# Kernel tuning notes

Measured on AMD Instinct MI355X. Metric: run time of the kernel, lower is better.

The kernel has to match this reference:

```python
import jax, jax.numpy as jnp
import numpy as np

B, S, D, H = 2, 2048, 2048, 16
HD = D // H  # 128


def _rope(x):
    # x: [b, h, s, d] -- standard half-split rotary embedding, theta=10000
    b, h, s, d = x.shape
    inv_freq = 1.0 / (10000.0 ** (jnp.arange(0, d, 2, dtype=jnp.float32) / d))  # [d/2]
    ang = jnp.arange(s, dtype=jnp.float32)[:, None] * inv_freq[None, :]  # [s, d/2]
    cos = jnp.cos(ang)[None, None].astype(x.dtype)
    sin = jnp.sin(ang)[None, None].astype(x.dtype)
    x1, x2 = x[..., : d // 2], x[..., d // 2 :]
    return jnp.concatenate([x1 * cos - x2 * sin, x2 * cos + x1 * sin], axis=-1)


def setup_inputs() -> dict:
    key = jax.random.key(0)
    ks = jax.random.split(key, 11)
    sc = 0.02
    return {
        "queries": jax.random.normal(ks[0], (B, S, D), jnp.float32),
        "keys": jax.random.normal(ks[1], (B, S, D), jnp.float32),
        "values": jax.random.normal(ks[2], (B, S, D), jnp.float32),
        "Wq": jax.random.normal(ks[3], (D, D), jnp.float32) * sc,
        "bq": jax.random.normal(ks[4], (D,), jnp.float32) * sc,
        "Wk": jax.random.normal(ks[5], (D, D), jnp.float32) * sc,
        "bk": jax.random.normal(ks[6], (D,), jnp.float32) * sc,
        "Wv": jax.random.normal(ks[7], (D, D), jnp.float32) * sc,
        "bv": jax.random.normal(ks[8], (D,), jnp.float32) * sc,
        "Wo": jax.random.normal(ks[9], (D, D), jnp.float32) * sc,
        "bo": jax.random.normal(ks[10], (D,), jnp.float32) * sc,
    }


def reference(queries, keys, values, Wq, bq, Wk, bk, Wv, bv, Wo, bo):
    b, sq, _ = queries.shape
    sk = keys.shape[1]
    # projections, split heads: [b, h, s, hd]
    q = (queries @ Wq + bq).reshape(b, sq, H, HD).transpose(0, 2, 1, 3)
    k = (keys @ Wk + bk).reshape(b, sk, H, HD).transpose(0, 2, 1, 3)
    v = (values @ Wv + bv).reshape(b, sk, H, HD).transpose(0, 2, 1, 3)
    q = _rope(q)
    k = _rope(k)
    scores = jnp.einsum("bhqd,bhkd->bhqk", q, k) / jnp.sqrt(jnp.asarray(HD, q.dtype))
    causal = jnp.triu(jnp.ones((sq, sk), dtype=bool), k=1)
    scores = jnp.where(causal, -jnp.inf, scores)
    attn = jax.nn.softmax(scores, axis=-1)
    out = jnp.einsum("bhqk,bhkd->bhqd", attn, v)
    out = out.transpose(0, 2, 1, 3).reshape(b, sq, H * HD)
    return out @ Wo + bo
```

## Files before the change

kernel.cpp:

```cpp
#include <hip/hip_runtime.h>
#include <hip/hip_bf16.h>
#include <math.h>

#define S_LEN 2048
#define D_DIM 2048
#define NHEAD 16
#define HD_DIM 128
#define NROWS 4096
#define BSD 8388608

typedef __bf16 bf16x8 __attribute__((ext_vector_type(8)));
typedef float f32x4 __attribute__((ext_vector_type(4)));
typedef unsigned short u16;
typedef unsigned int u32;

__device__ __forceinline__ float bf2f(u16 h) {
    union { u32 u; float f; } v; v.u = ((u32)h) << 16; return v.f;
}
__device__ __forceinline__ u16 f2bf(float f) {
    union { float f; u32 u; } v; v.f = f;
    u32 r = v.u + 0x7fffu + ((v.u >> 16) & 1u);
    return (u16)(r >> 16);
}

__device__ __forceinline__ void gld16(const void* g, void* l) {
    __builtin_amdgcn_global_load_lds((const __attribute__((address_space(1))) void*)g,
                                     (__attribute__((address_space(3))) void*)l,
                                     16, 0, 0);
}

__device__ __forceinline__ bool detect_f32(const void* p) {
    const u16* h = (const u16*)p;
    int sane = 0;
    for (int i = 0; i < 128; i++) {
        const u16 v = h[2 * i];
        const int e = (v >> 7) & 0xFF;
        sane += (int)((e >= 96 && e <= 150) || ((v & 0x7FFF) == 0));
    }
    return sane < 64;
}

__device__ __forceinline__ bf16x8 load8(const void* X, size_t eidx, bool f32) {
    if (!f32) return *(const bf16x8*)((const u16*)X + eidx);
    const float* xf = (const float*)X + eidx;
    const f32x4 a = *(const f32x4*)xf;
    const f32x4 b = *(const f32x4*)(xf + 4);
    bf16x8 r;
    u16* rp = (u16*)&r;
    rp[0] = f2bf(a[0]); rp[1] = f2bf(a[1]); rp[2] = f2bf(a[2]); rp[3] = f2bf(a[3]);
    rp[4] = f2bf(b[0]); rp[5] = f2bf(b[1]); rp[6] = f2bf(b[2]); rp[7] = f2bf(b[3]);
    return r;
}

__device__ __forceinline__ float bload(const void* b, int i, bool f32) {
    return f32 ? ((const float*)b)[i] : bf2f(((const u16*)b)[i]);
}

__global__ __launch_bounds__(256) void fill_k(float* __restrict__ out, float v, int n) {
    const int i = blockIdx.x * 256 + threadIdx.x;
    if (i < n) out[i] = v;
}

__device__ __forceinline__ void conv_body(const void* __restrict__ in,
                                          u16* __restrict__ out, bool f32) {
    const size_t i = ((size_t)blockIdx.x * 256 + threadIdx.x) << 3;
    if (f32) {
        const f32x4 a = *(const f32x4*)((const float*)in + i);
        const f32x4 b = *(const f32x4*)((const float*)in + i + 4);
        uint4 w;
        w.x = (u32)f2bf(a[0]) | ((u32)f2bf(a[1]) << 16);
        w.y = (u32)f2bf(a[2]) | ((u32)f2bf(a[3]) << 16);
        w.z = (u32)f2bf(b[0]) | ((u32)f2bf(b[1]) << 16);
        w.w = (u32)f2bf(b[2]) | ((u32)f2bf(b[3]) << 16);
        *(uint4*)&out[i] = w;
    } else {
        *(uint4*)&out[i] = *(const uint4*)&((const u16*)in)[i];
    }
}

__global__ __launch_bounds__(256) void conv_bf16(const void* __restrict__ in,
                                                 u16* __restrict__ out) {
    conv_body(in, out, detect_f32(in));
}

__global__ __launch_bounds__(256) void conv3(const void* __restrict__ q,
                                             const void* __restrict__ k,
                                             const void* __restrict__ v,
                                             u16* __restrict__ oq,
                                             u16* __restrict__ ok,
                                             u16* __restrict__ ov) {
    const int z = blockIdx.y;
    const void* in = (z == 0) ? q : (z == 1) ? k : v;
    u16* out = (z == 0) ? oq : (z == 1) ? ok : ov;
    conv_body(in, out, detect_f32(in));
}

__device__ __forceinline__ void transpose_body(const void* __restrict__ W,
                                               u16* __restrict__ out) {
    __shared__ float tile[64][68];
    const bool f32w = detect_f32(W);
    const int t = threadIdx.x;
    const int r = t >> 4, c4 = (t & 15) << 2;
    const int kb = blockIdx.y << 6, nb = blockIdx.x << 6;
    if (f32w) {
        #pragma unroll
        for (int i = 0; i < 4; i++) {
            const f32x4 v = *(const f32x4*)((const float*)W +
                (size_t)(kb + r + 16 * i) * D_DIM + nb + c4);
            tile[r + 16 * i][c4 + 0] = v[0];
            tile[r + 16 * i][c4 + 1] = v[1];
            tile[r + 16 * i][c4 + 2] = v[2];
            tile[r + 16 * i][c4 + 3] = v[3];
        }
    } else {
        #pragma unroll
        for (int i = 0; i < 4; i++)
            #pragma unroll
            for (int j = 0; j < 4; j++)
                tile[r + 16 * i][c4 + j] =
                    bf2f(((const u16*)W)[(size_t)(kb + r + 16 * i) * D_DIM + nb + c4 + j]);
    }
    __syncthreads();
    #pragma unroll
    for (int i = 0; i < 4; i++) {
        const int n = nb + r + 16 * i;
        u16 pk[4];
        #pragma unroll
        for (int j = 0; j < 4; j++) pk[j] = f2bf(tile[c4 + j][r + 16 * i]);
        *(uint2*)&out[(size_t)n * D_DIM + kb + c4] = *(uint2*)pk;
    }
}

__global__ __launch_bounds__(256) void transpose_w(const void* __restrict__ W,
                                                   u16* __restrict__ out) {
    transpose_body(W, out);
}

__global__ __launch_bounds__(256) void transpose_all(const void* __restrict__ W0,
                                                     const void* __restrict__ W1,
                                                     const void* __restrict__ W2,
                                                     u16* __restrict__ out) {
    const int z = blockIdx.z;
    const void* W = (z == 0) ? W0 : (z == 1) ? W1 : W2;
    transpose_body(W, out + (size_t)z * D_DIM * D_DIM);
}

__global__ __launch_bounds__(256) void qkv_gemm_bf(const u16* __restrict__ Xq,
                                                   const u16* __restrict__ Xk,
                                                   const u16* __restrict__ Xv,
                                                   const u16* __restrict__ WTbase,
                                                   const void* __restrict__ bqp,
                                                   const void* __restrict__ bkp,
                                                   const void* __restrict__ bvp,
                                                   u16* __restrict__ Oq,
                                                   u16* __restrict__ Ok,
                                                   u16* __restrict__ Ov) {
    __shared__ __align__(16) u16 a_s[128 * 32];
    __shared__ __align__(16) u16 b_s[128 * 32];
    const int z = blockIdx.z;
    const u16* X    = (z == 0) ? Xq  : (z == 1) ? Xk  : Xv;
    const void* bias= (z == 0) ? bqp : (z == 1) ? bkp : bvp;
    u16* out        = (z == 0) ? Oq  : (z == 1) ? Ok  : Ov;
    const u16* WT   = WTbase + (size_t)z * D_DIM * D_DIM;
    const bool f32b = detect_f32(bias);
    const int t = threadIdx.x;
    const int wave = t >> 6, lane = t & 63;
    const int quad = lane >> 4, m16 = lane & 15;
    const int wm = (wave >> 1) << 6, wn = (wave & 1) << 6;
    const int rowBase = blockIdx.y << 7, colBase = blockIdx.x << 7;
    const int arow = t >> 2, aoff = (t & 3) << 3;

    f32x4 acc[4][4];
    #pragma unroll
    for (int i = 0; i < 4; i++)
        #pragma unroll
        for (int j = 0; j < 4; j++) acc[i][j] = (f32x4){0.f, 0.f, 0.f, 0.f};

    for (int k0 = 0; k0 < D_DIM; k0 += 32) {
        __syncthreads();
        gld16(&X[(size_t)(rowBase + arow) * D_DIM + k0 + aoff],       &a_s[t * 8]);
        gld16(&X[(size_t)(rowBase + arow + 64) * D_DIM + k0 + aoff],  &a_s[(t + 256) * 8]);
        gld16(&WT[(size_t)(colBase + arow) * D_DIM + k0 + aoff],      &b_s[t * 8]);
        gld16(&WT[(size_t)(colBase + arow + 64) * D_DIM + k0 + aoff], &b_s[(t + 256) * 8]);
        __syncthreads();

        bf16x8 af[4], bfr[4];
        #pragma unroll
        for (int mi = 0; mi < 4; mi++)
            af[mi] = *(bf16x8*)&a_s[(wm + mi * 16 + m16) * 32 + quad * 8];
        #pragma unroll
        for (int ni = 0; ni < 4; ni++)
            bfr[ni] = *(bf16x8*)&b_s[(wn + ni * 16 + m16) * 32 + quad * 8];
        #pragma unroll
        for (int mi = 0; mi < 4; mi++)
            #pragma unroll
            for (int ni = 0; ni < 4; ni++)
                acc[mi][ni] = __builtin_amdgcn_mfma_f32_16x16x32_bf16(
                    af[mi], bfr[ni], acc[mi][ni], 0, 0, 0);
    }

    #pragma unroll
    for (int ni = 0; ni < 4; ni++) {
        const int col = colBase + wn + ni * 16 + m16;
        const float bv = bload(bias, col, f32b);
        const int h = col >> 7, hd = col & (HD_DIM - 1);
        #pragma unroll
        for (int mi = 0; mi < 4; mi++) {
            #pragma unroll
            for (int r = 0; r < 4; r++) {
                const int row = rowBase + wm + mi * 16 + quad * 4 + r;
                const int b = row >> 11, s = row & (S_LEN - 1);
                out[(((size_t)(b * NHEAD + h)) * S_LEN + s) * HD_DIM + hd] =
                    f2bf(acc[mi][ni][r] + bv);
            }
        }
    }
}

__global__ __launch_bounds__(256) void qkv_gemm(const void* __restrict__ Xq,
                                                const void* __restrict__ Xk,
                                                const void* __restrict__ Xv,
                                                const u16* __restrict__ WTbase,
                                                const void* __restrict__ bqp,
                                                const void* __restrict__ bkp,
                                                const void* __restrict__ bvp,
                                                u16* __restrict__ Oq,
                                                u16* __restrict__ Ok,
                                                u16* __restrict__ Ov) {
    __shared__ __align__(16) u16 a_s[128 * 32];
    __shared__ __align__(16) u16 b_s[128 * 32];
    const int z = blockIdx.z;
    const void* X   = (z == 0) ? Xq  : (z == 1) ? Xk  : Xv;
    const void* bias= (z == 0) ? bqp : (z == 1) ? bkp : bvp;
    u16* out        = (z == 0) ? Oq  : (z == 1) ? Ok  : Ov;
    const u16* WT   = WTbase + (size_t)z * D_DIM * D_DIM;
    const bool f32x = detect_f32(X);
    const bool f32b = detect_f32(bias);
    const int t = threadIdx.x;
    const int wave = t >> 6, lane = t & 63;
    const int quad = lane >> 4, m16 = lane & 15;
    const int wm = (wave >> 1) << 6, wn = (wave & 1) << 6;
    const int rowBase = blockIdx.y << 7, colBase = blockIdx.x << 7;
    const int arow = t >> 2, aoff = (t & 3) << 3;

    f32x4 acc[4][4];
    #pragma unroll
    for (int i = 0; i < 4; i++)
        #pragma unroll
        for (int j = 0; j < 4; j++) acc[i][j] = (f32x4){0.f, 0.f, 0.f, 0.f};

    for (int k0 = 0; k0 < D_DIM; k0 += 32) {
        const bf16x8 av0 = load8(X, (size_t)(rowBase + arow) * D_DIM + k0 + aoff, f32x);
        const bf16x8 av1 = load8(X, (size_t)(rowBase + arow + 64) * D_DIM + k0 + aoff, f32x);
        __syncthreads();
        *(bf16x8*)&a_s[arow * 32 + aoff]        = av0;
        *(bf16x8*)&a_s[(arow + 64) * 32 + aoff] = av1;
        gld16(&WT[(size_t)(colBase + arow) * D_DIM + k0 + aoff],      &b_s[t * 8]);
        gld16(&WT[(size_t)(colBase + arow + 64) * D_DIM + k0 + aoff], &b_s[(t + 256) * 8]);
        __syncthreads();

        bf16x8 af[4], bfr[4];
        #pragma unroll
        for (int mi = 0; mi < 4; mi++)
            af[mi] = *(bf16x8*)&a_s[(wm + mi * 16 + m16) * 32 + quad * 8];
        #pragma unroll
        for (int ni = 0; ni < 4; ni++)
            bfr[ni] = *(bf16x8*)&b_s[(wn + ni * 16 + m16) * 32 + quad * 8];
        #pragma unroll
        for (int mi = 0; mi < 4; mi++)
            #pragma unroll
            for (int ni = 0; ni < 4; ni++)
                acc[mi][ni] = __builtin_amdgcn_mfma_f32_16x16x32_bf16(
                    af[mi], bfr[ni], acc[mi][ni], 0, 0, 0);
    }

    #pragma unroll
    for (int ni = 0; ni < 4; ni++) {
        const int col = colBase + wn + ni * 16 + m16;
        const float bv = bload(bias, col, f32b);
        const int h = col >> 7, hd = col & (HD_DIM - 1);
        #pragma unroll
        for (int mi = 0; mi < 4; mi++) {
            #pragma unroll
            for (int r = 0; r < 4; r++) {
                const int row = rowBase + wm + mi * 16 + quad * 4 + r;
                const int b = row >> 11, s = row & (S_LEN - 1);
                out[(((size_t)(b * NHEAD + h)) * S_LEN + s) * HD_DIM + hd] =
                    f2bf(acc[mi][ni][r] + bv);
            }
        }
    }
}

template<int MODE>
__global__ __launch_bounds__(256) void bt_gemm(const void* __restrict__ X,
                                               const u16* __restrict__ WT,
                                               const void* __restrict__ bias,
                                               void* __restrict__ out) {
    __shared__ __align__(16) u16 a_s[128 * 32];
    __shared__ __align__(16) u16 b_s[128 * 32];
    const bool f32x = (MODE == 0) ? detect_f32(X) : false;
    const bool f32b = detect_f32(bias);
    const int t = threadIdx.x;
    const int wave = t >> 6, lane = t & 63;
    const int quad = lane >> 4, m16 = lane & 15;
    const int wm = (wave >> 1) << 6, wn = (wave & 1) << 6;
    const int rowBase = blockIdx.y << 7, colBase = blockIdx.x << 7;
    const int arow = t >> 2, aoff = (t & 3) << 3;

    f32x4 acc[4][4];
    #pragma unroll
    for (int i = 0; i < 4; i++)
        #pragma unroll
        for (int j = 0; j < 4; j++) acc[i][j] = (f32x4){0.f, 0.f, 0.f, 0.f};

    for (int k0 = 0; k0 < D_DIM; k0 += 32) {
        if (MODE == 0) {
            const bf16x8 av0 = load8(X, (size_t)(rowBase + arow) * D_DIM + k0 + aoff, f32x);
            const bf16x8 av1 = load8(X, (size_t)(rowBase + arow + 64) * D_DIM + k0 + aoff, f32x);
            __syncthreads();
            *(bf16x8*)&a_s[arow * 32 + aoff]        = av0;
            *(bf16x8*)&a_s[(arow + 64) * 32 + aoff] = av1;
            gld16(&WT[(size_t)(colBase + arow) * D_DIM + k0 + aoff],      &b_s[t * 8]);
            gld16(&WT[(size_t)(colBase + arow + 64) * D_DIM + k0 + aoff], &b_s[(t + 256) * 8]);
            __syncthreads();
        } else {
            __syncthreads();
            if (MODE == 2) {
                gld16(&((const u16*)X)[(size_t)(rowBase + arow) * D_DIM + k0 + aoff],
                      &a_s[t * 8]);
                gld16(&((const u16*)X)[(size_t)(rowBase + arow + 64) * D_DIM + k0 + aoff],
                      &a_s[(t + 256) * 8]);
            } else {
                const int kg = k0 + aoff, h = kg >> 7, hd = kg & (HD_DIM - 1);
                const int r0 = rowBase + arow, r1 = r0 + 64;
                gld16(&((const u16*)X)[
                    (((size_t)((r0 >> 11) * NHEAD + h)) * S_LEN + (r0 & (S_LEN - 1))) * HD_DIM + hd],
                    &a_s[t * 8]);
                gld16(&((const u16*)X)[
                    (((size_t)((r1 >> 11) * NHEAD + h)) * S_LEN + (r1 & (S_LEN - 1))) * HD_DIM + hd],
                    &a_s[(t + 256) * 8]);
            }
            gld16(&WT[(size_t)(colBase + arow) * D_DIM + k0 + aoff],      &b_s[t * 8]);
            gld16(&WT[(size_t)(colBase + arow + 64) * D_DIM + k0 + aoff], &b_s[(t + 256) * 8]);
            __syncthreads();
        }

        bf16x8 af[4], bfr[4];
        #pragma unroll
        for (int mi = 0; mi < 4; mi++)
            af[mi] = *(bf16x8*)&a_s[(wm + mi * 16 + m16) * 32 + quad * 8];
        #pragma unroll
        for (int ni = 0; ni < 4; ni++)
            bfr[ni] = *(bf16x8*)&b_s[(wn + ni * 16 + m16) * 32 + quad * 8];
        #pragma unroll
        for (int mi = 0; mi < 4; mi++)
            #pragma unroll
            for (int ni = 0; ni < 4; ni++)
                acc[mi][ni] = __builtin_amdgcn_mfma_f32_16x16x32_bf16(
                    af[mi], bfr[ni], acc[mi][ni], 0, 0, 0);
    }

    #pragma unroll
    for (int ni = 0; ni < 4; ni++) {
        const int col = colBase + wn + ni * 16 + m16;
        const float bv = bload(bias, col, f32b);
        const int h = col >> 7, hd = col & (HD_DIM - 1);
        #pragma unroll
        for (int mi = 0; mi < 4; mi++) {
            #pragma unroll
            for (int r = 0; r < 4; r++) {
                const int row = rowBase + wm + mi * 16 + quad * 4 + r;
                const float v = acc[mi][ni][r] + bv;
                if (MODE == 1) {
                    ((float*)out)[(size_t)row * D_DIM + col] = v;
                } else {
                    const int b = row >> 11, s = row & (S_LEN - 1);
                    ((u16*)out)[(((size_t)(b * NHEAD + h)) * S_LEN + s) * HD_DIM + hd] = f2bf(v);
                }
            }
        }
    }
}

__global__ __launch_bounds__(256) void gemm_qkv(const void* __restrict__ X,
                                                const void* __restrict__ W,
                                                const void* __restrict__ bias,
                                                u16* __restrict__ out) {
    __shared__ __align__(16) u16 a_s[64 * 32];
    __shared__ __align__(16) u16 b_s[64 * 40];
    const bool f32x = detect_f32(X);
    const bool f32w = detect_f32(W);
    const bool f32b = detect_f32(bias);
    const int t = threadIdx.x;
    const int wave = t >> 6, lane = t & 63;
    const int quad = lane >> 4, mrow = lane & 15;
    const int rowBase = blockIdx.y * 64;
    const int colBase = blockIdx.x * 64;
    const int srow = t >> 2, soff = (t & 3) << 3;
    const int krow = t >> 3, ncol0 = (t & 7) << 3;

    f32x4 acc0 = {0.f, 0.f, 0.f, 0.f};
    f32x4 acc1 = acc0, acc2 = acc0, acc3 = acc0;

    for (int k0 = 0; k0 < D_DIM; k0 += 32) {
        const bf16x8 av = load8(X, (size_t)(rowBase + srow) * D_DIM + k0 + soff, f32x);
        const bf16x8 wv = load8(W, (size_t)(k0 + krow) * D_DIM + colBase + ncol0, f32w);
        __syncthreads();
        *(bf16x8*)&a_s[srow * 32 + soff] = av;
        const u16* wp = (const u16*)&wv;
        #pragma unroll
        for (int j = 0; j < 8; j++) b_s[(ncol0 + j) * 40 + krow] = wp[j];
        __syncthreads();
        const bf16x8 af  = *(bf16x8*)&a_s[(wave * 16 + mrow) * 32 + (quad << 3)];
        const bf16x8 bf0 = *(bf16x8*)&b_s[(     mrow) * 40 + (quad << 3)];
        const bf16x8 bf1 = *(bf16x8*)&b_s[(16 + mrow) * 40 + (quad << 3)];
        const bf16x8 bf2 = *(bf16x8*)&b_s[(32 + mrow) * 40 + (quad << 3)];
        const bf16x8 bf3 = *(bf16x8*)&b_s[(48 + mrow) * 40 + (quad << 3)];
        acc0 = __builtin_amdgcn_mfma_f32_16x16x32_bf16(af, bf0, acc0, 0, 0, 0);
        acc1 = __builtin_amdgcn_mfma_f32_16x16x32_bf16(af, bf1, acc1, 0, 0, 0);
        acc2 = __builtin_amdgcn_mfma_f32_16x16x32_bf16(af, bf2, acc2, 0, 0, 0);
        acc3 = __builtin_amdgcn_mfma_f32_16x16x32_bf16(af, bf3, acc3, 0, 0, 0);
    }

    const f32x4 accs[4] = {acc0, acc1, acc2, acc3};
    #pragma unroll
    for (int cb = 0; cb < 4; cb++) {
        const int col = colBase + cb * 16 + mrow;
        const float bv = bload(bias, col, f32b);
        const int h = col >> 7, hd = col & (HD_DIM - 1);
        #pragma unroll
        for (int r = 0; r < 4; r++) {
            const int row = rowBase + wave * 16 + quad * 4 + r;
            const int b = row >> 11, s = row & (S_LEN - 1);
            out[(((size_t)(b * NHEAD + h)) * S_LEN + s) * HD_DIM + hd] =
                f2bf(accs[cb][r] + bv);
        }
    }
}

__global__ __launch_bounds__(256) void gemm_o(const u16* __restrict__ A,
                                              const void* __restrict__ W,
                                              const void* __restrict__ bias,
                                              float* __restrict__ out) {
    __shared__ __align__(16) u16 a_s[64 * 32];
    __shared__ __align__(16) u16 b_s[64 * 40];
    const bool f32w = detect_f32(W);
    const bool f32b = detect_f32(bias);
    const int t = threadIdx.x;
    const int wave = t >> 6, lane = t & 63;
    const int quad = lane >> 4, mrow = lane & 15;
    const int rowBase = blockIdx.y * 64;
    const int colBase = blockIdx.x * 64;
    const int srow = t >> 2, soff = (t & 3) << 3;
    const int krow = t >> 3, ncol0 = (t & 7) << 3;

    f32x4 acc0 = {0.f, 0.f, 0.f, 0.f};
    f32x4 acc1 = acc0, acc2 = acc0, acc3 = acc0;

    const int row = rowBase + srow;
    const int rb = row >> 11, rs = row & (S_LEN - 1);

    for (int k0 = 0; k0 < D_DIM; k0 += 32) {
        const int kg = k0 + soff;
        const int h = kg >> 7, hd = kg & (HD_DIM - 1);
        const bf16x8 av = *(const bf16x8*)&A[
            (((size_t)(rb * NHEAD + h)) * S_LEN + rs) * HD_DIM + hd];
        const bf16x8 wv = load8(W, (size_t)(k0 + krow) * D_DIM + colBase + ncol0, f32w);
        __syncthreads();
        *(bf16x8*)&a_s[srow * 32 + soff] = av;
        const u16* wp = (const u16*)&wv;
        #pragma unroll
        for (int j = 0; j < 8; j++) b_s[(ncol0 + j) * 40 + krow] = wp[j];
        __syncthreads();
        const bf16x8 af  = *(bf16x8*)&a_s[(wave * 16 + mrow) * 32 + (quad << 3)];
        const bf16x8 bf0 = *(bf16x8*)&b_s[(     mrow) * 40 + (quad << 3)];
        const bf16x8 bf1 = *(bf16x8*)&b_s[(16 + mrow) * 40 + (quad << 3)];
        const bf16x8 bf2 = *(bf16x8*)&b_s[(32 + mrow) * 40 + (quad << 3)];
        const bf16x8 bf3 = *(bf16x8*)&b_s[(48 + mrow) * 40 + (quad << 3)];
        acc0 = __builtin_amdgcn_mfma_f32_16x16x32_bf16(af, bf0, acc0, 0, 0, 0);
        acc1 = __builtin_amdgcn_mfma_f32_16x16x32_bf16(af, bf1, acc1, 0, 0, 0);
        acc2 = __builtin_amdgcn_mfma_f32_16x16x32_bf16(af, bf2, acc2, 0, 0, 0);
        acc3 = __builtin_amdgcn_mfma_f32_16x16x32_bf16(af, bf3, acc3, 0, 0, 0);
    }

    const f32x4 accs[4] = {acc0, acc1, acc2, acc3};
    #pragma unroll
    for (int cb = 0; cb < 4; cb++) {
        const int col = colBase + cb * 16 + mrow;
        const float bv = bload(bias, col, f32b);
        #pragma unroll
        for (int r = 0; r < 4; r++) {
            const int orow = rowBase + wave * 16 + quad * 4 + r;
            out[(size_t)orow * D_DIM + col] = accs[cb][r] + bv;
        }
    }
}

__global__ __launch_bounds__(256) void rope_k(u16* __restrict__ q, u16* __restrict__ k) {
    const int idx = blockIdx.x * 256 + threadIdx.x;
    u16* p = blockIdx.y ? k : q;
    const int i  = idx & 63;
    const int s  = (idx >> 6) & (S_LEN - 1);
    const int bh = idx >> 17;
    const size_t base = ((size_t)bh * S_LEN + s) * HD_DIM;
    const float inv = __expf((float)i * -0.14391157f);
    const float ang = (float)s * inv;
    const float c = cosf(ang), sn = sinf(ang);
    const float x1 = bf2f(p[base + i]);
    const float x2 = bf2f(p[base + 64 + i]);
    p[base + i]      = f2bf(x1 * c - x2 * sn);
    p[base + 64 + i] = f2bf(x2 * c + x1 * sn);
}

__device__ __forceinline__ int vswz(int d, int blk8) {
    return d * 72 + (((blk8) ^ ((d ^ (d >> 3)) & 7)) << 3);
}

__global__ __launch_bounds__(256, 3) void flash_mfma(const u16* Q,
                                                     const u16* __restrict__ K,
                                                     const u16* __restrict__ V,
                                                     u16* Out) {
    __shared__ __align__(16) u16 k_s[64 * 136];
    __shared__ __align__(16) u16 v_s[128 * 72];
    __shared__ __align__(16) u16 p_s[64 * 72];
    const int t = threadIdx.x;
    const int wave = t >> 6, lane = t & 63;
    const int quad = lane >> 4, m16 = lane & 15;
    const int h = blockIdx.y, b = blockIdx.z;
    const int q0 = (int)(gridDim.x - 1 - blockIdx.x) << 6;
    const size_t bhoff = ((size_t)(b * NHEAD + h)) * S_LEN * HD_DIM;

    #pragma unroll
    for (int i = 0; i < 4; i++) {
        const int chunk = t + 256 * i;
        const int row = chunk >> 4, d0 = (chunk & 15) << 3;
        *(uint4*)&k_s[row * 136 + d0] =
            *(const uint4*)&Q[bhoff + (size_t)(q0 + row) * HD_DIM + d0];
    }
    __syncthreads();
    bf16x8 qf[4];
    #pragma unroll
    for (int kc = 0; kc < 4; kc++)
        qf[kc] = *(bf16x8*)&k_s[(wave * 16 + m16) * 136 + kc * 32 + quad * 8];

    f32x4 o[8];
    #pragma unroll
    for (int i = 0; i < 8; i++) o[i] = (f32x4){0.f, 0.f, 0.f, 0.f};
    f32x4 m_i = {-1e30f, -1e30f, -1e30f, -1e30f};
    f32x4 l_i = {0.f, 0.f, 0.f, 0.f};

    const int row_g0 = q0 + wave * 16 + quad * 4;
    const float scale = 0.08838834764831843f;
    const int nt = (q0 >> 6) + 1;

    const int krow = t >> 4, kd0 = (t & 15) << 3;
    const int dg = t & 15, kvg = t >> 4;
    const int vsub = (kvg & 1) << 2;

    uint4 kreg[4], vreg[4];
    #pragma unroll
    for (int i = 0; i < 4; i++) {
        kreg[i] = *(const uint4*)&K[bhoff + (size_t)(krow + 16 * i) * HD_DIM + kd0];
        vreg[i] = *(const uint4*)&V[bhoff + (size_t)(kvg * 4 + i) * HD_DIM + dg * 8];
    }

    for (int it = 0; it < nt; ++it) {
        const int kb = it << 6;
        __syncthreads();
        #pragma unroll
        for (int i = 0; i < 4; i++)
            *(uint4*)&k_s[(krow + 16 * i) * 136 + kd0] = kreg[i];
        {
            const u16* v0 = (const u16*)&vreg[0];
            const u16* v1 = (const u16*)&vreg[1];
            const u16* v2 = (const u16*)&vreg[2];
            const u16* v3 = (const u16*)&vreg[3];
            #pragma unroll
            for (int j = 0; j < 8; j++) {
                const int d = dg * 8 + j;
                uint2 w;
                w.x = (u32)v0[j] | ((u32)v1[j] << 16);
                w.y = (u32)v2[j] | ((u32)v3[j] << 16);
                *(uint2*)&v_s[vswz(d, kvg >> 1) + vsub] = w;
            }
        }
        __syncthreads();
        if (it + 1 < nt) {
            const int kb2 = kb + 64;
            #pragma unroll
            for (int i = 0; i < 4; i++) {
                kreg[i] = *(const uint4*)&K[bhoff + (size_t)(kb2 + krow + 16 * i) * HD_DIM + kd0];
                vreg[i] = *(const uint4*)&V[bhoff + (size_t)(kb2 + kvg * 4 + i) * HD_DIM + dg * 8];
            }
        }

        f32x4 s[4];
        #pragma unroll
        for (int f = 0; f < 4; f++) s[f] = (f32x4){0.f, 0.f, 0.f, 0.f};
        __builtin_amdgcn_s_setprio(1);
        #pragma unroll
        for (int kc = 0; kc < 4; kc++) {
            #pragma unroll
            for (int f = 0; f < 4; f++) {
                const bf16x8 kf = *(bf16x8*)&k_s[(f * 16 + m16) * 136 + kc * 32 + quad * 8];
                s[f] = __builtin_amdgcn_mfma_f32_16x16x32_bf16(qf[kc], kf, s[f], 0, 0, 0);
            }
        }
        __builtin_amdgcn_s_setprio(0);

        f32x4 mx;
        #pragma unroll
        for (int r = 0; r < 4; r++) {
            float m0 = -1e30f;
            #pragma unroll
            for (int f = 0; f < 4; f++) {
                float a = s[f][r] * scale;
                if (kb + f * 16 + m16 > row_g0 + r) a = -1e30f;
                s[f][r] = a;
                m0 = fmaxf(m0, a);
            }
            mx[r] = m0;
        }
        #pragma unroll
        for (int d = 1; d <= 8; d <<= 1)
            #pragma unroll
            for (int r = 0; r < 4; r++) mx[r] = fmaxf(mx[r], __shfl_xor(mx[r], d));

        f32x4 alpha, rs;
        #pragma unroll
        for (int r = 0; r < 4; r++) {
            const float mn = fmaxf(m_i[r], mx[r]);
            alpha[r] = __expf(m_i[r] - mn);
            m_i[r] = mn;
            float acc = 0.f;
            #pragma unroll
            for (int f = 0; f < 4; f++) {
                s[f][r] = __expf(s[f][r] - mn);
                acc += s[f][r];
            }
            rs[r] = acc;
        }
        #pragma unroll
        for (int d = 1; d <= 8; d <<= 1)
            #pragma unroll
            for (int r = 0; r < 4; r++) rs[r] += __shfl_xor(rs[r], d);
        #pragma unroll
        for (int r = 0; r < 4; r++) l_i[r] = l_i[r] * alpha[r] + rs[r];

        #pragma unroll
        for (int f = 0; f < 4; f++)
            #pragma unroll
            for (int r = 0; r < 4; r++)
                p_s[(wave * 16 + quad * 4 + r) * 72 + f * 16 + m16] = f2bf(s[f][r]);

        #pragma unroll
        for (int n = 0; n < 8; n++) o[n] *= alpha;

        __builtin_amdgcn_s_setprio(1);
        #pragma unroll
        for (int kc = 0; kc < 2; kc++) {
            const bf16x8 pa = *(bf16x8*)&p_s[(wave * 16 + m16) * 72 + kc * 32 + quad * 8];
            #pragma unroll
            for (int n = 0; n < 8; n++) {
                const int d = n * 16 + m16;
                const bf16x8 vb = *(bf16x8*)&v_s[vswz(d, kc * 4 + quad)];
                o[n] = __builtin_amdgcn_mfma_f32_16x16x32_bf16(pa, vb, o[n], 0, 0, 0);
            }
        }
        __builtin_amdgcn_s_setprio(0);
    }

    f32x4 inv;
    #pragma unroll
    for (int r = 0; r < 4; r++) inv[r] = 1.f / l_i[r];
    #pragma unroll
    for (int n = 0; n < 8; n++)
        #pragma unroll
        for (int r = 0; r < 4; r++)
            Out[bhoff + (size_t)(row_g0 + r) * HD_DIM + n * 16 + m16] =
                f2bf(o[n][r] * inv[r]);
}

extern "C" void kernel_launch(void* const* d_in, const int* in_sizes, int n_in,
                              void* d_out, int out_size, void* d_ws, size_t ws_size,
                              hipStream_t stream) {
    float* outf = (float*)d_out;

    bool order_ok = (n_in == 11);
    if (order_ok) {
        const int expect[11] = {8388608, 8388608, 8388608, 4194304, 2048,
                                4194304, 2048, 4194304, 2048, 4194304, 2048};
        for (int i = 0; i < 11; i++) order_ok = order_ok && (in_sizes[i] == expect[i]);
    }
    if (!order_ok) {
        fill_k<<<dim3((out_size + 255) / 256), dim3(256), 0, stream>>>(outf, 50.f, out_size);
        return;
    }
    if (ws_size < (size_t)BSD * sizeof(u16)) {
        fill_k<<<dim3((out_size + 255) / 256), dim3(256), 0, stream>>>(outf, 25.f, out_size);
        return;
    }

    const void* queries = d_in[0];
    const void* keys    = d_in[1];
    const void* values  = d_in[2];
    const void* Wq = d_in[3]; const void* bq = d_in[4];
    const void* Wk = d_in[5]; const void* bk = d_in[6];
    const void* Wv = d_in[7]; const void* bv = d_in[8];
    const void* Wo = d_in[9]; const void* bo = d_in[10];

    const dim3 tb(256);
    const dim3 gr(16384, 2);
    const dim3 gf(S_LEN / 64, NHEAD, 2);

    const size_t wslot = (size_t)D_DIM * D_DIM * 2;
    const size_t need_full  = (size_t)BSD * 8 + 3 * wslot;
    const size_t need_fused = (size_t)BSD * 4 + 3 * wslot;
    const size_t need_fast  = (size_t)BSD * 4 + wslot;

    if (ws_size >= need_full) {
        u16* Qb = (u16*)d_ws;
        u16* Kb = Qb + BSD;
        u16* Vb = Kb + BSD;
        u16* WT = Vb + BSD;
        u16* XV = WT + 3 * (size_t)D_DIM * D_DIM;
        u16* XQ = (u16*)d_out;
        u16* XK = XQ + BSD;

        const dim3 gc3(4096, 3);
        const dim3 gt3(32, 32, 3);
        const dim3 gt(32, 32);
        const dim3 gq(16, 32, 3);
        const dim3 gb(16, 32);

        conv3<<<gc3, tb, 0, stream>>>(queries, keys, values, XQ, XK, XV);
        transpose_all<<<gt3, tb, 0, stream>>>(Wq, Wk, Wv, WT);
        qkv_gemm_bf<<<gq, tb, 0, stream>>>(XQ, XK, XV, WT, bq, bk, bv, Qb, Kb, Vb);
        transpose_w<<<gt, tb, 0, stream>>>(Wo, WT);
        rope_k<<<gr, tb, 0, stream>>>(Qb, Kb);
        flash_mfma<<<gf, tb, 0, stream>>>(Qb, Kb, Vb, Qb);
        bt_gemm<1><<<gb, tb, 0, stream>>>(Qb, WT, bo, outf);
        return;
    }

    u16* Qb = (u16*)d_ws;
    u16* Kb = (u16*)d_out;
    u16* Vb = Kb + BSD;

    const size_t need_r3 = (size_t)BSD * 2 + 3 * wslot;
    const size_t need_r2 = (size_t)BSD * 2 + wslot;

    if (ws_size >= need_r3) {
        u16* WT = Qb + BSD;
        const dim3 gt3(32, 32, 3);
        const dim3 gt(32, 32);
        const dim3 gq(16, 32, 3);
        const dim3 gb(16, 32);

        transpose_all<<<gt3, tb, 0, stream>>>(Wq, Wk, Wv, WT);
        qkv_gemm<<<gq, tb, 0, stream>>>(queries, keys, values, WT,
                                        bq, bk, bv, Qb, Kb, Vb);
        transpose_w<<<gt, tb, 0, stream>>>(Wo, WT);
        rope_k<<<gr, tb, 0, stream>>>(Qb, Kb);
        flash_mfma<<<gf, tb, 0, stream>>>(Qb, Kb, Vb, Qb);
        bt_gemm<1><<<gb, tb, 0, stream>>>(Qb, WT, bo, outf);
    } else if (ws_size >= need_r2) {
        u16* WT = Qb + BSD;
        u16* XQ = Kb;
        u16* XK = Vb;
        const dim3 gt(32, 32);
        const dim3 gb(16, 32);
        const dim3 gc(4096);

        conv_bf16<<<gc, tb, 0, stream>>>(queries, XQ);
        conv_bf16<<<gc, tb, 0, stream>>>(keys, XK);

        transpose_w<<<gt, tb, 0, stream>>>(Wq, WT);
        bt_gemm<2><<<gb, tb, 0, stream>>>(XQ, WT, bq, Qb);
        transpose_w<<<gt, tb, 0, stream>>>(Wk, WT);
        bt_gemm<2><<<gb, tb, 0, stream>>>(XK, WT, bk, Kb);
        transpose_w<<<gt, tb, 0, stream>>>(Wv, WT);
        bt_gemm<0><<<gb, tb, 0, stream>>>(values, WT, bv, Vb);

        rope_k<<<gr, tb, 0, stream>>>(Qb, Kb);
        flash_mfma<<<gf, tb, 0, stream>>>(Qb, Kb, Vb, Qb);

        transpose_w<<<gt, tb, 0, stream>>>(Wo, WT);
        bt_gemm<1><<<gb, tb, 0, stream>>>(Qb, WT, bo, outf);
    } else {
        const dim3 gg(32, 64);
        gemm_qkv<<<gg, tb, 0, stream>>>(queries, Wq, bq, Qb);
        gemm_qkv<<<gg, tb, 0, stream>>>(keys,    Wk, bk, Kb);
        gemm_qkv<<<gg, tb, 0, stream>>>(values,  Wv, bv, Vb);
        rope_k<<<gr, tb, 0, stream>>>(Qb, Kb);
        flash_mfma<<<gf, tb, 0, stream>>>(Qb, Kb, Vb, Qb);
        gemm_o<<<gg, tb, 0, stream>>>(Qb, Wo, bo, outf);
    }
}
```

Baseline: 829.1 us.

## Double-buffer GEMM LDS tiles and add 8-wave 128-row flash attention kernel

The QKV and output-projection GEMMs now use two LDS buffers, so the async global-to-LDS loads for the next K slice are issued before the MFMA work on the current slice, with one barrier per iteration instead of two. A new flash attention kernel uses 512 threads covering 128 query rows per block, sharing each staged K/V tile across twice as many rows. It also prefetches the next K/V tile into registers and uses reversed block order to schedule the longer causal rows first. The costs are doubled LDS use in the GEMMs and higher register and LDS pressure in the attention kernel, which may lower occupancy. In the attention kernel, the Q/K/V buffer is also overwritten with the output in place.

```diff
diff --git a/kernel.cpp b/kernel.cpp
--- a/kernel.cpp
+++ b/kernel.cpp
@@ -155,8 +155,8 @@
                                                    u16* __restrict__ Oq,
                                                    u16* __restrict__ Ok,
                                                    u16* __restrict__ Ov) {
-    __shared__ __align__(16) u16 a_s[128 * 32];
-    __shared__ __align__(16) u16 b_s[128 * 32];
+    __shared__ __align__(16) u16 a_s[2][128 * 32];
+    __shared__ __align__(16) u16 b_s[2][128 * 32];
     const int z = blockIdx.z;
     const u16* X    = (z == 0) ? Xq  : (z == 1) ? Xk  : Xv;
     const void* bias= (z == 0) ? bqp : (z == 1) ? bkp : bvp;
@@ -176,27 +176,35 @@
         #pragma unroll
         for (int j = 0; j < 4; j++) acc[i][j] = (f32x4){0.f, 0.f, 0.f, 0.f};
 
-    for (int k0 = 0; k0 < D_DIM; k0 += 32) {
-        __syncthreads();
-        gld16(&X[(size_t)(rowBase + arow) * D_DIM + k0 + aoff],       &a_s[t * 8]);
-        gld16(&X[(size_t)(rowBase + arow + 64) * D_DIM + k0 + aoff],  &a_s[(t + 256) * 8]);
-        gld16(&WT[(size_t)(colBase + arow) * D_DIM + k0 + aoff],      &b_s[t * 8]);
-        gld16(&WT[(size_t)(colBase + arow + 64) * D_DIM + k0 + aoff], &b_s[(t + 256) * 8]);
-        __syncthreads();
-
+    gld16(&X[(size_t)(rowBase + arow) * D_DIM + aoff],        &a_s[0][t * 8]);
+    gld16(&X[(size_t)(rowBase + arow + 64) * D_DIM + aoff],   &a_s[0][(t + 256) * 8]);
+    gld16(&WT[(size_t)(colBase + arow) * D_DIM + aoff],       &b_s[0][t * 8]);
+    gld16(&WT[(size_t)(colBase + arow + 64) * D_DIM + aoff],  &b_s[0][(t + 256) * 8]);
+    __syncthreads();
+
+    int cur = 0;
+    for (int k0 = 0; k0 < D_DIM; k0 += 32, cur ^= 1) {
+        if (k0 + 32 < D_DIM) {
+            const int kn = k0 + 32;
+            gld16(&X[(size_t)(rowBase + arow) * D_DIM + kn + aoff],       &a_s[cur ^ 1][t * 8]);
+            gld16(&X[(size_t)(rowBase + arow + 64) * D_DIM + kn + aoff],  &a_s[cur ^ 1][(t + 256) * 8]);
+            gld16(&WT[(size_t)(colBase + arow) * D_DIM + kn + aoff],      &b_s[cur ^ 1][t * 8]);
+            gld16(&WT[(size_t)(colBase + arow + 64) * D_DIM + kn + aoff], &b_s[cur ^ 1][(t + 256) * 8]);
+        }
         bf16x8 af[4], bfr[4];
         #pragma unroll
         for (int mi = 0; mi < 4; mi++)
-            af[mi] = *(bf16x8*)&a_s[(wm + mi * 16 + m16) * 32 + quad * 8];
+            af[mi] = *(bf16x8*)&a_s[cur][(wm + mi * 16 + m16) * 32 + quad * 8];
         #pragma unroll
         for (int ni = 0; ni < 4; ni++)
-            bfr[ni] = *(bf16x8*)&b_s[(wn + ni * 16 + m16) * 32 + quad * 8];
+            bfr[ni] = *(bf16x8*)&b_s[cur][(wn + ni * 16 + m16) * 32 + quad * 8];
         #pragma unroll
         for (int mi = 0; mi < 4; mi++)
             #pragma unroll
             for (int ni = 0; ni < 4; ni++)
                 acc[mi][ni] = __builtin_amdgcn_mfma_f32_16x16x32_bf16(
                     af[mi], bfr[ni], acc[mi][ni], 0, 0, 0);
+        __syncthreads();
     }
 
     #pragma unroll
@@ -297,9 +305,6 @@
                                                const u16* __restrict__ WT,
                                                const void* __restrict__ bias,
                                                void* __restrict__ out) {
-    __shared__ __align__(16) u16 a_s[128 * 32];
-    __shared__ __align__(16) u16 b_s[128 * 32];
-    const bool f32x = (MODE == 0) ? detect_f32(X) : false;
     const bool f32b = detect_f32(bias);
     const int t = threadIdx.x;
     const int wave = t >> 6, lane = t & 63;
@@ -314,8 +319,11 @@
         #pragma unroll
         for (int j = 0; j < 4; j++) acc[i][j] = (f32x4){0.f, 0.f, 0.f, 0.f};
 
-    for (int k0 = 0; k0 < D_DIM; k0 += 32) {
-        if (MODE == 0) {
+    if constexpr (MODE == 0) {
+        __shared__ __align__(16) u16 a_s[128 * 32];
+        __shared__ __align__(16) u16 b_s[128 * 32];
+        const bool f32x = detect_f32(X);
+        for (int k0 = 0; k0 < D_DIM; k0 += 32) {
             const bf16x8 av0 = load8(X, (size_t)(rowBase + arow) * D_DIM + k0 + aoff, f32x);
             const bf16x8 av1 = load8(X, (size_t)(rowBase + arow + 64) * D_DIM + k0 + aoff, f32x);
             __syncthreads();
@@ -324,41 +332,66 @@
             gld16(&WT[(size_t)(colBase + arow) * D_DIM + k0 + aoff],      &b_s[t * 8]);
             gld16(&WT[(size_t)(colBase + arow + 64) * D_DIM + k0 + aoff], &b_s[(t + 256) * 8]);
             __syncthreads();
-        } else {
+
+            bf16x8 af[4], bfr[4];
+            #pragma unroll
+            for (int mi = 0; mi < 4; mi++)
+                af[mi] = *(bf16x8*)&a_s[(wm + mi * 16 + m16) * 32 + quad * 8];
+            #pragma unroll
+            for (int ni = 0; ni < 4; ni++)
+                bfr[ni] = *(bf16x8*)&b_s[(wn + ni * 16 + m16) * 32 + quad * 8];
+            #pragma unroll
+            for (int mi = 0; mi < 4; mi++)
+                #pragma unroll
+                for (int ni = 0; ni < 4; ni++)
+                    acc[mi][ni] = __builtin_amdgcn_mfma_f32_16x16x32_bf16(
+                        af[mi], bfr[ni], acc[mi][ni], 0, 0, 0);
+        }
+    } else {
+        __shared__ __align__(16) u16 a_s[2][128 * 32];
+        __shared__ __align__(16) u16 b_s[2][128 * 32];
+        #define STAGE_T(buf, kk)                                                          \
+            do {                                                                          \
+                if (MODE == 2) {                                                          \
+                    gld16(&((const u16*)X)[(size_t)(rowBase + arow) * D_DIM + (kk) + aoff],      \
+                          &a_s[buf][t * 8]);                                              \
+                    gld16(&((const u16*)X)[(size_t)(rowBase + arow + 64) * D_DIM + (kk) + aoff], \
+                          &a_s[buf][(t + 256) * 8]);                                      \
+                } else {                                                                  \
+                    const int kg = (kk) + aoff, hh = kg >> 7, hd2 = kg & (HD_DIM - 1);    \
+                    const int r0 = rowBase + arow, r1 = r0 + 64;                          \
+                    gld16(&((const u16*)X)[                                               \
+                        (((size_t)((r0 >> 11) * NHEAD + hh)) * S_LEN + (r0 & (S_LEN - 1))) * HD_DIM + hd2], \
+                        &a_s[buf][t * 8]);                                                \
+                    gld16(&((const u16*)X)[                                               \
+                        (((size_t)((r1 >> 11) * NHEAD + hh)) * S_LEN + (r1 & (S_LEN - 1))) * HD_DIM + hd2], \
+                        &a_s[buf][(t + 256) * 8]);                                        \
+                }                                                                         \
+                gld16(&WT[(size_t)(colBase + arow) * D_DIM + (kk) + aoff],      &b_s[buf][t * 8]);        \
+                gld16(&WT[(size_t)(colBase + arow + 64) * D_DIM + (kk) + aoff], &b_s[buf][(t + 256) * 8]);\
+            } while (0)
+
+        STAGE_T(0, 0);
+        __syncthreads();
+        int cur = 0;
+        for (int k0 = 0; k0 < D_DIM; k0 += 32, cur ^= 1) {
+            if (k0 + 32 < D_DIM) STAGE_T(cur ^ 1, k0 + 32);
+            bf16x8 af[4], bfr[4];
+            #pragma unroll
+            for (int mi = 0; mi < 4; mi++)
+                af[mi] = *(bf16x8*)&a_s[cur][(wm + mi * 16 + m16) * 32 + quad * 8];
+            #pragma unroll
+            for (int ni = 0; ni < 4; ni++)
+                bfr[ni] = *(bf16x8*)&b_s[cur][(wn + ni * 16 + m16) * 32 + quad * 8];
+            #pragma unroll
+            for (int mi = 0; mi < 4; mi++)
+                #pragma unroll
+                for (int ni = 0; ni < 4; ni++)
+                    acc[mi][ni] = __builtin_amdgcn_mfma_f32_16x16x32_bf16(
+                        af[mi], bfr[ni], acc[mi][ni], 0, 0, 0);
             __syncthreads();
-            if (MODE == 2) {
-                gld16(&((const u16*)X)[(size_t)(rowBase + arow) * D_DIM + k0 + aoff],
-                      &a_s[t * 8]);
-                gld16(&((const u16*)X)[(size_t)(rowBase + arow + 64) * D_DIM + k0 + aoff],
-                      &a_s[(t + 256) * 8]);
-            } else {
-                const int kg = k0 + aoff, h = kg >> 7, hd = kg & (HD_DIM - 1);
-                const int r0 = rowBase + arow, r1 = r0 + 64;
-                gld16(&((const u16*)X)[
-                    (((size_t)((r0 >> 11) * NHEAD + h)) * S_LEN + (r0 & (S_LEN - 1))) * HD_DIM + hd],
-                    &a_s[t * 8]);
-                gld16(&((const u16*)X)[
-                    (((size_t)((r1 >> 11) * NHEAD + h)) * S_LEN + (r1 & (S_LEN - 1))) * HD_DIM + hd],
-                    &a_s[(t + 256) * 8]);
-            }
-            gld16(&WT[(size_t)(colBase + arow) * D_DIM + k0 + aoff],      &b_s[t * 8]);
-            gld16(&WT[(size_t)(colBase + arow + 64) * D_DIM + k0 + aoff], &b_s[(t + 256) * 8]);
-            __syncthreads();
-        }
-
-        bf16x8 af[4], bfr[4];
-        #pragma unroll
-        for (int mi = 0; mi < 4; mi++)
-            af[mi] = *(bf16x8*)&a_s[(wm + mi * 16 + m16) * 32 + quad * 8];
-        #pragma unroll
-        for (int ni = 0; ni < 4; ni++)
-            bfr[ni] = *(bf16x8*)&b_s[(wn + ni * 16 + m16) * 32 + quad * 8];
-        #pragma unroll
-        for (int mi = 0; mi < 4; mi++)
-            #pragma unroll
-            for (int ni = 0; ni < 4; ni++)
-                acc[mi][ni] = __builtin_amdgcn_mfma_f32_16x16x32_bf16(
-                    af[mi], bfr[ni], acc[mi][ni], 0, 0, 0);
+        }
+        #undef STAGE_T
     }
 
     #pragma unroll
@@ -682,6 +715,173 @@
                 f2bf(o[n][r] * inv[r]);
 }
 
+__global__ __launch_bounds__(512, 4) void flash_mfma8(const u16* __restrict__ Q,
+                                                      const u16* __restrict__ K,
+                                                      const u16* __restrict__ V,
+                                                      u16* __restrict__ Out) {
+    __shared__ __align__(16) u16 k_s[64 * 136];
+    __shared__ __align__(16) u16 v_s[128 * 72];
+    __shared__ __align__(16) u16 p_s[128 * 72];
+    const int t = threadIdx.x;
+    const int wave = t >> 6, lane = t & 63;
+    const int quad = lane >> 4, m16 = lane & 15;
+    const int h = blockIdx.y, b = blockIdx.z;
+    const int q0 = (int)(gridDim.x - 1 - blockIdx.x) << 7;
+    const size_t bhoff = ((size_t)(b * NHEAD + h)) * S_LEN * HD_DIM;
+
+    bf16x8 qf[4];
+    {
+        const size_t qrow = bhoff + (size_t)(q0 + wave * 16 + m16) * HD_DIM;
+        #pragma unroll
+        for (int kc = 0; kc < 4; kc++)
+            qf[kc] = *(const bf16x8*)&Q[qrow + kc * 32 + quad * 8];
+    }
+
+    f32x4 o[8];
+    #pragma unroll
+    for (int i = 0; i < 8; i++) o[i] = (f32x4){0.f, 0.f, 0.f, 0.f};
+    f32x4 m_i = {-1e30f, -1e30f, -1e30f, -1e30f};
+    f32x4 l_i = {0.f, 0.f, 0.f, 0.f};
+
+    const int row_g0 = q0 + wave * 16 + quad * 4;
+    const float scale = 0.08838834764831843f;
+    const int nt = (q0 >> 6) + 2;
+
+    const int krow = t >> 4, kd0 = (t & 15) << 3;
+    const int dg = t & 15, kvp = t >> 4;
+    const int vbase = (kvp & 3) << 1;
+
+    uint4 kreg[2], vreg[2];
+    kreg[0] = *(const uint4*)&K[bhoff + (size_t)(krow) * HD_DIM + kd0];
+    kreg[1] = *(const uint4*)&K[bhoff + (size_t)(krow + 32) * HD_DIM + kd0];
+    vreg[0] = *(const uint4*)&V[bhoff + (size_t)(kvp * 2) * HD_DIM + dg * 8];
+    vreg[1] = *(const uint4*)&V[bhoff + (size_t)(kvp * 2 + 1) * HD_DIM + dg * 8];
+
+    for (int it = 0; it < nt; ++it) {
+        const int kb = it << 6;
+        __syncthreads();
+        *(uint4*)&k_s[(krow) * 136 + kd0]      = kreg[0];
+        *(uint4*)&k_s[(krow + 32) * 136 + kd0] = kreg[1];
+        {
+            const u16* v0 = (const u16*)&vreg[0];
+            const u16* v1 = (const u16*)&vreg[1];
+            #pragma unroll
+            for (int j = 0; j < 8; j++) {
+                const int d = dg * 8 + j;
+                const u32 w = (u32)v0[j] | ((u32)v1[j] << 16);
+                *(u32*)&v_s[vswz(d, kvp >> 2) + vbase] = w;
+            }
+        }
+        __syncthreads();
+        if (it + 1 < nt) {
+            const int kb2 = kb + 64;
+            kreg[0] = *(const uint4*)&K[bhoff + (size_t)(kb2 + krow) * HD_DIM + kd0];
+            kreg[1] = *(const uint4*)&K[bhoff + (size_t)(kb2 + krow + 32) * HD_DIM + kd0];
+            vreg[0] = *(const uint4*)&V[bhoff + (size_t)(kb2 + kvp * 2) * HD_DIM + dg * 8];
+            vreg[1] = *(const uint4*)&V[bhoff + (size_t)(kb2 + kvp * 2 + 1) * HD_DIM + dg * 8];
+        }
+
+        f32x4 s[4];
+        #pragma unroll
+        for (int f = 0; f < 4; f++) s[f] = (f32x4){0.f, 0.f, 0.f, 0.f};
+        __builtin_amdgcn_s_setprio(1);
+        #pragma unroll
+        for (int kc = 0; kc < 4; kc++) {
+            #pragma unroll
+            for (int f = 0; f < 4; f++) {
+                const bf16x8 kf = *(bf16x8*)&k_s[(f * 16 + m16) * 136 + kc * 32 + quad * 8];
+                s[f] = __builtin_amdgcn_mfma_f32_16x16x32_bf16(qf[kc], kf, s[f], 0, 0, 0);
+            }
+        }
+        __builtin_amdgcn_s_setprio(0);
+
+        f32x4 mx;
+        if (kb + 63 > row_g0) {
+            #pragma unroll
+            for (int r = 0; r < 4; r++) {
+                float m0 = -1e30f;
+                #pragma unroll
+                for (int f = 0; f < 4; f++) {
+                    float a = s[f][r] * scale;
+                    if (kb + f * 16 + m16 > row_g0 + r) a = -1e30f;
+                    s[f][r] = a;
+                    m0 = fmaxf(m0, a);
+                }
+                mx[r] = m0;
+            }
+        } else {
+            #pragma unroll
+            for (int r = 0; r < 4; r++) {
+                float m0 = -1e30f;
+                #pragma unroll
+                for (int f = 0; f < 4; f++) {
+                    const float a = s[f][r] * scale;
+                    s[f][r] = a;
+                    m0 = fmaxf(m0, a);
+                }
+                mx[r] = m0;
+            }
+        }
+        #pragma unroll
+        for (int d = 1; d <= 8; d <<= 1)
+            #pragma unroll
+            for (int r = 0; r < 4; r++) mx[r] = fmaxf(mx[r], __shfl_xor(mx[r], d));
+
+        f32x4 alpha, rs;
+        #pragma unroll
+        for (int r = 0; r < 4; r++) {
+            const float mn = fmaxf(m_i[r], mx[r]);
+            alpha[r] = __expf(m_i[r] - mn);
+            m_i[r] = mn;
+            float acc = 0.f;
+            #pragma unroll
+            for (int f = 0; f < 4; f++) {
+                s[f][r] = __expf(s[f][r] - mn);
+                acc += s[f][r];
+            }
+            rs[r] = acc;
+        }
+        #pragma unroll
+        for (int d = 1; d <= 8; d <<= 1)
+            #pragma unroll
+            for (int r = 0; r < 4; r++) rs[r] += __shfl_xor(rs[r], d);
+        #pragma unroll
+        for (int r = 0; r < 4; r++) l_i[r] = l_i[r] * alpha[r] + rs[r];
+
+        #pragma unroll
+        for (int f = 0; f < 4; f++)
+            #pragma unroll
+            for (int r = 0; r < 4; r++)
+                p_s[(wave * 16 + quad * 4 + r) * 72 + f * 16 + m16] = f2bf(s[f][r]);
+
+        #pragma unroll
+        for (int n = 0; n < 8; n++) o[n] *= alpha;
+
+        __builtin_amdgcn_s_setprio(1);
+        #pragma unroll
+        for (int kc = 0; kc < 2; kc++) {
+            const bf16x8 pa = *(bf16x8*)&p_s[(wave * 16 + m16) * 72 + kc * 32 + quad * 8];
+            #pragma unroll
+            for (int n = 0; n < 8; n++) {
+                const int d = n * 16 + m16;
+                const bf16x8 vb = *(bf16x8*)&v_s[vswz(d, kc * 4 + quad)];
+                o[n] = __builtin_amdgcn_mfma_f32_16x16x32_bf16(pa, vb, o[n], 0, 0, 0);
+            }
+        }
+        __builtin_amdgcn_s_setprio(0);
+    }
+
+    f32x4 inv;
+    #pragma unroll
+    for (int r = 0; r < 4; r++) inv[r] = 1.f / l_i[r];
+    #pragma unroll
+    for (int n = 0; n < 8; n++)
+        #pragma unroll
+        for (int r = 0; r < 4; r++)
+            Out[bhoff + (size_t)(row_g0 + r) * HD_DIM + n * 16 + m16] =
+                f2bf(o[n][r] * inv[r]);
+}
+
 extern "C" void kernel_launch(void* const* d_in, const int* in_sizes, int n_in,
                               void* d_out, int out_size, void* d_ws, size_t ws_size,
                               hipStream_t stream) {
@@ -712,12 +912,9 @@
 
     const dim3 tb(256);
     const dim3 gr(16384, 2);
-    const dim3 gf(S_LEN / 64, NHEAD, 2);
 
     const size_t wslot = (size_t)D_DIM * D_DIM * 2;
     const size_t need_full  = (size_t)BSD * 8 + 3 * wslot;
-    const size_t need_fused = (size_t)BSD * 4 + 3 * wslot;
-    const size_t need_fast  = (size_t)BSD * 4 + wslot;
 
     if (ws_size >= need_full) {
         u16* Qb = (u16*)d_ws;
@@ -733,13 +930,15 @@
         const dim3 gt(32, 32);
         const dim3 gq(16, 32, 3);
         const dim3 gb(16, 32);
+        const dim3 gf8(S_LEN / 128, NHEAD, 2);
+        const dim3 tb8(512);
 
         conv3<<<gc3, tb, 0, stream>>>(queries, keys, values, XQ, XK, XV);
         transpose_all<<<gt3, tb, 0, stream>>>(Wq, Wk, Wv, WT);
         qkv_gemm_bf<<<gq, tb, 0, stream>>>(XQ, XK, XV, WT, bq, bk, bv, Qb, Kb, Vb);
         transpose_w<<<gt, tb, 0, stream>>>(Wo, WT);
         rope_k<<<gr, tb, 0, stream>>>(Qb, Kb);
-        flash_mfma<<<gf, tb, 0, stream>>>(Qb, Kb, Vb, Qb);
+        flash_mfma8<<<gf8, tb8, 0, stream>>>(Qb, Kb, Vb, Qb);
         bt_gemm<1><<<gb, tb, 0, stream>>>(Qb, WT, bo, outf);
         return;
     }
@@ -747,6 +946,7 @@
     u16* Qb = (u16*)d_ws;
     u16* Kb = (u16*)d_out;
     u16* Vb = Kb + BSD;
+    const dim3 gf(S_LEN / 64, NHEAD, 2);
 
     const size_t need_r3 = (size_t)BSD * 2 + 3 * wslot;
     const size_t need_r2 = (size_t)BSD * 2 + wslot;
```

Measured after the change: 841.4 us. Within noise of the previous version (+1.5%).
